# Kernel optimization log

Measured on AMD Instinct MI355X. Metric: run time of the kernel, lower is better.

## Reference

```python
import jax, jax.numpy as jnp
import numpy as np

HEADS = 8
DIM_HEAD = 64
SCALE = DIM_HEAD ** -0.5


def setup_inputs() -> dict:
    key = jax.random.key(0)
    k1, k2, k3, k4 = jax.random.split(key, 4)
    b, c, f, h, w = 2, 512, 16, 32, 32
    x = jax.random.normal(k1, (b, c, f, h, w), dtype=jnp.float32)
    pos_bias = jax.random.normal(k2, (HEADS, f, f), dtype=jnp.float32)
    # torch Linear(dim, 3*hidden, bias=False): store as (in, out) for right-matmul
    w_qkv = jax.random.normal(k3, (c, 3 * HEADS * DIM_HEAD), dtype=jnp.float32) * (c ** -0.5)
    w_out = jax.random.normal(k4, (HEADS * DIM_HEAD, c), dtype=jnp.float32) * ((HEADS * DIM_HEAD) ** -0.5)
    return {"x": x, "pos_bias": pos_bias, "w_qkv": w_qkv, "w_out": w_out}


def reference(x, pos_bias, w_qkv, w_out):
    b, c, f, h, w = x.shape
    # 'b c f h w -> (b h w) f c'
    xt = jnp.transpose(x, (0, 3, 4, 2, 1)).reshape(b * h * w, f, c)
    qkv = xt @ w_qkv  # (B, f, 3*hidden)
    q, k, v = jnp.split(qkv, 3, axis=-1)
    def to_heads(t):  # (B, f, h*d) -> (B, heads, f, d)
        return t.reshape(t.shape[0], f, HEADS, DIM_HEAD).transpose(0, 2, 1, 3)
    q, k, v = to_heads(q) * SCALE, to_heads(k), to_heads(v)
    sim = jnp.einsum('bhid,bhjd->bhij', q, k)
    sim = sim + pos_bias  # (heads, f, f) broadcasts over batch
    attn = jax.nn.softmax(sim, axis=-1)  # stable max-subtract softmax
    out = jnp.einsum('bhij,bhjd->bhid', attn, v)
    out = out.transpose(0, 2, 1, 3).reshape(b * h * w, f, HEADS * DIM_HEAD)
    out = out @ w_out  # (B, f, c)
    # '(b h w) f c -> b c f h w'
    return out.reshape(b, h, w, f, c).transpose(0, 4, 3, 1, 2)
```

## Files before the change

kernel.cpp:

```cpp
#include <hip/hip_runtime.h>

typedef unsigned short u16;
typedef unsigned int u32;
typedef __attribute__((ext_vector_type(8))) short short8;
typedef __attribute__((ext_vector_type(4))) float f32x4;

__device__ __forceinline__ u16 f2bf(float f) {
  u32 u = __builtin_bit_cast(u32, f);
  u += 0x7fffu + ((u >> 16) & 1u);
  return (u16)(u >> 16);
}

__device__ __forceinline__ void async16(const void* g, void* l) {
  __builtin_amdgcn_global_load_lds(
      (const __attribute__((address_space(1))) u32*)g,
      (__attribute__((address_space(3))) u32*)l, 16, 0, 0);
}

__global__ __launch_bounds__(256) void k_wt(const float* __restrict__ in,
                                            u16* __restrict__ outT,
                                            int K, int N, int scaleN, int perm) {
  const int bid = blockIdx.x;
  const int ntiles = N >> 5;
  const int nt = bid % ntiles, kt = bid / ntiles;
  const int n0 = nt << 5, k0 = kt << 5;
  __shared__ float tile[32][33];
  const int t = threadIdx.x;
#pragma unroll
  for (int i = 0; i < 4; ++i) {
    const int e = t + i * 256, r = e >> 5, c = e & 31;
    tile[c][r] = in[(size_t)(k0 + r) * N + n0 + c];
  }
  __syncthreads();
#pragma unroll
  for (int i = 0; i < 4; ++i) {
    const int e = t + i * 256, r = e >> 5, c = e & 31;
    float v = tile[r][c];
    if (n0 + r < scaleN) v *= 0.125f;
    const int kcol = k0 + c;
    const int kp = perm ? ((kcol & ~63) | ((kcol & 15) << 2) | ((kcol >> 4) & 3))
                        : kcol;
    outT[(size_t)(n0 + r) * K + kp] = f2bf(v);
  }
}

__global__ __launch_bounds__(256) void k_xt(const float* __restrict__ x,
                                            u16* __restrict__ XT) {
  const int bid = blockIdx.x;
  const int plane = bid & 31;
  const int rest = bid >> 5;
  const int mt = rest & 31, ct = rest >> 5;
  const int bb = plane >> 4, f = plane & 15;
  const int m0 = mt << 5, c0 = ct << 5;
  __shared__ float tile[32][33];
  const int t = threadIdx.x;
#pragma unroll
  for (int i = 0; i < 4; ++i) {
    const int e = t + i * 256, r = e >> 5, c = e & 31;
    tile[c][r] = x[((size_t)((bb * 512 + c0 + r) * 16 + f)) * 1024 + m0 + c];
  }
  __syncthreads();
#pragma unroll
  for (int i = 0; i < 4; ++i) {
    const int e = t + i * 256, r = e >> 5, c = e & 31;
    XT[((size_t)((bb * 1024 + m0 + r) * 16 + f)) * 512 + c0 + c] = f2bf(tile[r][c]);
  }
}

struct A3St { u16 A[128][64]; u16 B[192][64]; };
struct A3At { u16 q[8][16][64]; u16 k[8][16][64]; u16 vt[8][64][16]; u16 pad[16]; };
union A3Sm { A3St st; A3At at; };

__global__ __launch_bounds__(256) void k_qkv_attn(const u16* __restrict__ XT,
                                                  const u16* __restrict__ WQ,
                                                  const float* __restrict__ pos_bias,
                                                  u16* __restrict__ AO) {
  const int tid = threadIdx.x;
  const int w = tid >> 6, lane = tid & 63;
  const int c15 = lane & 15, quad = lane >> 4;
  const int bid = blockIdx.x;
  const int hd = bid & 7, m0 = (bid >> 3) << 7;

  __shared__ A3Sm sm;

  const int lr = lane >> 3, lcb = lane & 7;

  f32x4 acc[3][8];
#pragma unroll
  for (int c = 0; c < 3; ++c)
#pragma unroll
    for (int mt = 0; mt < 8; ++mt) acc[c][mt] = f32x4{0.f, 0.f, 0.f, 0.f};

  for (int kk = 0; kk < 8; ++kk) {
    __syncthreads();
    const int kc = kk << 6;
#pragma unroll
    for (int t2 = 0; t2 < 4; ++t2) {
      const int r = w * 32 + t2 * 8 + lr;
      const int swcol = kc + ((lcb ^ (r & 7)) << 3);
      async16(XT + (size_t)(m0 + r) * 512 + swcol, &sm.st.A[w * 32 + t2 * 8][0]);
    }
#pragma unroll
    for (int t2 = 0; t2 < 6; ++t2) {
      const int j = w * 48 + t2 * 8 + lr;
      const int grow = (j >> 6) * 512 + hd * 64 + (j & 63);
      const int swcol = kc + ((lcb ^ (j & 7)) << 3);
      async16(WQ + (size_t)grow * 512 + swcol, &sm.st.B[w * 48 + t2 * 8][0]);
    }
    __syncthreads();
#pragma unroll
    for (int half = 0; half < 2; ++half) {
      short8 af[8], bt[3];
#pragma unroll
      for (int mt = 0; mt < 8; ++mt) {
        const int row = mt * 16 + c15;
        const int swz = (((half << 2) + quad) ^ (row & 7)) << 3;
        af[mt] = *(const short8*)&sm.st.A[row][swz];
      }
#pragma unroll
      for (int c = 0; c < 3; ++c) {
        const int row = c * 64 + w * 16 + c15;
        const int swz = (((half << 2) + quad) ^ (row & 7)) << 3;
        bt[c] = *(const short8*)&sm.st.B[row][swz];
      }
#pragma unroll
      for (int c = 0; c < 3; ++c)
#pragma unroll
        for (int mt = 0; mt < 8; ++mt)
          acc[c][mt] = __builtin_amdgcn_mfma_f32_16x16x32_bf16(af[mt], bt[c], acc[c][mt], 0, 0, 0);
    }
  }
  __syncthreads();

  const int dloc = w * 16 + c15;
  const int ch_b = dloc >> 3, dl = dloc & 7;
#pragma unroll
  for (int mt = 0; mt < 8; ++mt) {
#pragma unroll
    for (int r = 0; r < 4; ++r) {
      const int f = quad * 4 + r;
      const int sw = ((ch_b ^ (f & 7)) << 3) | dl;
      sm.at.q[mt][f][sw] = f2bf(acc[0][mt][r]);
      sm.at.k[mt][f][sw] = f2bf(acc[1][mt][r]);
      sm.at.vt[mt][dloc][f] = f2bf(acc[2][mt][r]);
    }
  }
  __syncthreads();

  float pb[4];
#pragma unroll
  for (int r = 0; r < 4; ++r)
    pb[r] = pos_bias[hd * 256 + (quad * 4 + r) * 16 + c15];

  for (int sblk = 0; sblk < 2; ++sblk) {
    const int s = w * 2 + sblk;
    f32x4 sacc = f32x4{0.f, 0.f, 0.f, 0.f};
#pragma unroll
    for (int h = 0; h < 2; ++h) {
      const int chunk = (((h << 2) + quad) ^ (c15 & 7)) << 3;
      const short8 aq = *(const short8*)&sm.at.q[s][c15][chunk];
      const short8 bk = *(const short8*)&sm.at.k[s][c15][chunk];
      sacc = __builtin_amdgcn_mfma_f32_16x16x32_bf16(aq, bk, sacc, 0, 0, 0);
    }
    asm volatile("" ::: "memory");
    u16* lp = &sm.at.q[s][0][0];
#pragma unroll
    for (int e = 0; e < 4; ++e) lp[c15 * 32 + 16 + quad * 4 + e] = 0;
#pragma unroll
    for (int r = 0; r < 4; ++r) {
      float sv = sacc[r] + pb[r];
      float mx = sv;
      mx = fmaxf(mx, __shfl_xor(mx, 1));
      mx = fmaxf(mx, __shfl_xor(mx, 2));
      mx = fmaxf(mx, __shfl_xor(mx, 4));
      mx = fmaxf(mx, __shfl_xor(mx, 8));
      const float e = __expf(sv - mx);
      float sum = e;
      sum += __shfl_xor(sum, 1);
      sum += __shfl_xor(sum, 2);
      sum += __shfl_xor(sum, 4);
      sum += __shfl_xor(sum, 8);
      lp[(quad * 4 + r) * 32 + c15] = f2bf(e / sum);
    }
    asm volatile("" ::: "memory");
    const short8 ap = *(const short8*)&lp[c15 * 32 + quad * 8];
    f32x4 oacc[4];
#pragma unroll
    for (int t = 0; t < 4; ++t) {
      const short8 bv = *(const short8*)&sm.at.vt[s][t * 16 + c15][(quad & 1) * 8];
      oacc[t] = __builtin_amdgcn_mfma_f32_16x16x32_bf16(ap, bv, f32x4{0.f, 0.f, 0.f, 0.f}, 0, 0, 0);
    }
    const int s_g = (m0 >> 4) + s;
    const int bb = s_g >> 10, sp = s_g & 1023;
#pragma unroll
    for (int r = 0; r < 4; ++r) {
      union { u16 us[4]; uint2 v; } pk;
#pragma unroll
      for (int t = 0; t < 4; ++t) pk.us[t] = f2bf(oacc[t][r]);
      *(uint2*)(AO + ((size_t)(bb * 16384 + (quad * 4 + r) * 1024 + sp)) * 512 +
                hd * 64 + c15 * 4) = pk.v;
    }
  }
}

struct K2St { u16 A[128][64]; u16 B[128][64]; };
union K2Sm { K2St st; float C[64][130]; };

__global__ __launch_bounds__(256) void k_proj(const u16* __restrict__ AO,
                                              const u16* __restrict__ WO,
                                              float* __restrict__ out) {
  const int tid = threadIdx.x, w = tid >> 6, lane = tid & 63;
  const int c15 = lane & 15, quad = lane >> 4;
  const int bid = blockIdx.x;
  const int nb = bid & 3, mb = bid >> 2;
  const int m0 = mb << 7, n0 = nb << 7;
  const int b = m0 >> 14, mloc = m0 & 16383;
  __shared__ K2Sm sm;
  f32x4 acc[8][2];
#pragma unroll
  for (int mt = 0; mt < 8; ++mt) {
    acc[mt][0] = f32x4{0.f, 0.f, 0.f, 0.f};
    acc[mt][1] = f32x4{0.f, 0.f, 0.f, 0.f};
  }
  const int lr = lane >> 3, lcb = lane & 7;
  for (int kk = 0; kk < 8; ++kk) {
    __syncthreads();
    const int kc = kk << 6;
#pragma unroll
    for (int t2 = 0; t2 < 4; ++t2) {
      const int r = w * 32 + t2 * 8 + lr;
      const int swcol = kc + ((lcb ^ (r & 7)) << 3);
      async16(AO + (size_t)(m0 + r) * 512 + swcol, &sm.st.A[w * 32 + t2 * 8][0]);
      async16(WO + (size_t)(n0 + r) * 512 + swcol, &sm.st.B[w * 32 + t2 * 8][0]);
    }
    __syncthreads();
#pragma unroll
    for (int half = 0; half < 2; ++half) {
      short8 af[8], bt[2];
#pragma unroll
      for (int mt = 0; mt < 8; ++mt) {
        const int row = mt * 16 + c15;
        const int swz = (((half << 2) + quad) ^ (row & 7)) << 3;
        af[mt] = *(const short8*)&sm.st.A[row][swz];
      }
#pragma unroll
      for (int nt = 0; nt < 2; ++nt) {
        const int row = w * 32 + nt * 16 + c15;
        const int swz = (((half << 2) + quad) ^ (row & 7)) << 3;
        bt[nt] = *(const short8*)&sm.st.B[row][swz];
      }
#pragma unroll
      for (int mt = 0; mt < 8; ++mt) {
        acc[mt][0] = __builtin_amdgcn_mfma_f32_16x16x32_bf16(af[mt], bt[0], acc[mt][0], 0, 0, 0);
        acc[mt][1] = __builtin_amdgcn_mfma_f32_16x16x32_bf16(af[mt], bt[1], acc[mt][1], 0, 0, 0);
      }
    }
  }
  __syncthreads();
#pragma unroll
  for (int h = 0; h < 2; ++h) {
#pragma unroll
    for (int mt2 = 0; mt2 < 4; ++mt2) {
      const int mt = h * 4 + mt2;
#pragma unroll
      for (int nt = 0; nt < 2; ++nt)
#pragma unroll
        for (int r = 0; r < 4; ++r)
          sm.C[mt2 * 16 + quad * 4 + r][w * 32 + nt * 16 + c15] = acc[mt][nt][r];
    }
    __syncthreads();
    for (int jj = 0; jj < 32; ++jj) {
      const int ch = n0 + w * 32 + jj;
      out[(size_t)(b * 512 + ch) * 16384 + mloc + h * 64 + lane] = sm.C[lane][w * 32 + jj];
    }
    __syncthreads();
  }
}

extern "C" void kernel_launch(void* const* d_in, const int* in_sizes, int n_in,
                              void* d_out, int out_size, void* d_ws, size_t ws_size,
                              hipStream_t stream) {
  const float* x = (const float*)d_in[0];
  const float* pos_bias = (const float*)d_in[1];
  const float* w_qkv = (const float*)d_in[2];
  const float* w_out = (const float*)d_in[3];
  float* out = (float*)d_out;
  char* ws = (char*)d_ws;
  u16* XT = (u16*)(ws);
  u16* AO = (u16*)(ws + (size_t)33554432);
  u16* WQ = (u16*)(ws + (size_t)67108864);
  u16* WO = (u16*)(ws + (size_t)68681728);

  hipLaunchKernelGGL(k_wt, dim3(768), dim3(256), 0, stream, w_qkv, WQ, 512, 1536, 512, 0);
  hipLaunchKernelGGL(k_wt, dim3(256), dim3(256), 0, stream, w_out, WO, 512, 512, 0, 1);
  hipLaunchKernelGGL(k_xt, dim3(16384), dim3(256), 0, stream, x, XT);
  hipLaunchKernelGGL(k_qkv_attn, dim3(2048), dim3(256), 0, stream, XT, WQ, pos_bias, AO);
  hipLaunchKernelGGL(k_proj, dim3(1024), dim3(256), 0, stream, AO, WO, out);
}
```

Measured before the change: 246.2 us.

## Vectorize transpose, hoist load pointers, pack bf16 stores, reorder block indexing

The x transpose kernel now reads float4 per thread and writes packed 4-element bf16 stores instead of scalar accesses. Both GEMM kernels precompute swizzled global pointers outside the K loop and fully unroll it. V-transpose and output stores pack pairs of bf16 into 32/64-bit writes. The block-index mapping is swapped so consecutive blocks share the same head or output-column tile, changing weight reuse across concurrently running blocks. Full unrolling raises register pressure and code size.

```diff
diff --git a/kernel.cpp b/kernel.cpp
--- a/kernel.cpp
+++ b/kernel.cpp
@@ -2,6 +2,7 @@
 
 typedef unsigned short u16;
 typedef unsigned int u32;
+typedef unsigned long long u64;
 typedef __attribute__((ext_vector_type(8))) short short8;
 typedef __attribute__((ext_vector_type(4))) float f32x4;
 
@@ -9,6 +10,9 @@
   u32 u = __builtin_bit_cast(u32, f);
   u += 0x7fffu + ((u >> 16) & 1u);
   return (u16)(u >> 16);
+}
+__device__ __forceinline__ u32 pk2bf(float a, float b) {
+  return (u32)f2bf(a) | ((u32)f2bf(b) << 16);
 }
 
 __device__ __forceinline__ void async16(const void* g, void* l) {
@@ -52,19 +56,18 @@
   const int mt = rest & 31, ct = rest >> 5;
   const int bb = plane >> 4, f = plane & 15;
   const int m0 = mt << 5, c0 = ct << 5;
-  __shared__ float tile[32][33];
+  __shared__ float tile[32][36];
   const int t = threadIdx.x;
-#pragma unroll
-  for (int i = 0; i < 4; ++i) {
-    const int e = t + i * 256, r = e >> 5, c = e & 31;
-    tile[c][r] = x[((size_t)((bb * 512 + c0 + r) * 16 + f)) * 1024 + m0 + c];
-  }
-  __syncthreads();
-#pragma unroll
-  for (int i = 0; i < 4; ++i) {
-    const int e = t + i * 256, r = e >> 5, c = e & 31;
-    XT[((size_t)((bb * 1024 + m0 + r) * 16 + f)) * 512 + c0 + c] = f2bf(tile[r][c]);
-  }
+  const int lr = t >> 3, lc = t & 7;
+  const float4 v4 = *(const float4*)
+      &x[((size_t)((bb * 512 + c0 + lr) * 16 + f)) * 1024 + m0 + lc * 4];
+  *(float4*)&tile[lr][lc * 4] = v4;
+  __syncthreads();
+  const int m = t >> 3, cc = t & 7;
+  union { u32 uu[2]; u64 q; } pk;
+  pk.uu[0] = pk2bf(tile[cc * 4 + 0][m], tile[cc * 4 + 1][m]);
+  pk.uu[1] = pk2bf(tile[cc * 4 + 2][m], tile[cc * 4 + 3][m]);
+  *(u64*)&XT[((size_t)((bb * 1024 + m0 + m) * 16 + f)) * 512 + c0 + cc * 4] = pk.q;
 }
 
 struct A3St { u16 A[128][64]; u16 B[192][64]; };
@@ -79,34 +82,41 @@
   const int w = tid >> 6, lane = tid & 63;
   const int c15 = lane & 15, quad = lane >> 4;
   const int bid = blockIdx.x;
-  const int hd = bid & 7, m0 = (bid >> 3) << 7;
+  const int hd = bid >> 8, m0 = (bid & 255) << 7;
 
   __shared__ A3Sm sm;
 
   const int lr = lane >> 3, lcb = lane & 7;
 
+  const u16* aptr[4];
+  const u16* bptr[6];
+#pragma unroll
+  for (int t2 = 0; t2 < 4; ++t2) {
+    const int r = w * 32 + t2 * 8 + lr;
+    aptr[t2] = XT + (size_t)(m0 + r) * 512 + ((lcb ^ (r & 7)) << 3);
+  }
+#pragma unroll
+  for (int t2 = 0; t2 < 6; ++t2) {
+    const int j = w * 48 + t2 * 8 + lr;
+    const int grow = (j >> 6) * 512 + hd * 64 + (j & 63);
+    bptr[t2] = WQ + (size_t)grow * 512 + ((lcb ^ (j & 7)) << 3);
+  }
+
   f32x4 acc[3][8];
 #pragma unroll
   for (int c = 0; c < 3; ++c)
 #pragma unroll
     for (int mt = 0; mt < 8; ++mt) acc[c][mt] = f32x4{0.f, 0.f, 0.f, 0.f};
 
+#pragma unroll
   for (int kk = 0; kk < 8; ++kk) {
     __syncthreads();
-    const int kc = kk << 6;
-#pragma unroll
-    for (int t2 = 0; t2 < 4; ++t2) {
-      const int r = w * 32 + t2 * 8 + lr;
-      const int swcol = kc + ((lcb ^ (r & 7)) << 3);
-      async16(XT + (size_t)(m0 + r) * 512 + swcol, &sm.st.A[w * 32 + t2 * 8][0]);
-    }
-#pragma unroll
-    for (int t2 = 0; t2 < 6; ++t2) {
-      const int j = w * 48 + t2 * 8 + lr;
-      const int grow = (j >> 6) * 512 + hd * 64 + (j & 63);
-      const int swcol = kc + ((lcb ^ (j & 7)) << 3);
-      async16(WQ + (size_t)grow * 512 + swcol, &sm.st.B[w * 48 + t2 * 8][0]);
-    }
+#pragma unroll
+    for (int t2 = 0; t2 < 4; ++t2)
+      async16(aptr[t2] + (kk << 6), &sm.st.A[w * 32 + t2 * 8][0]);
+#pragma unroll
+    for (int t2 = 0; t2 < 6; ++t2)
+      async16(bptr[t2] + (kk << 6), &sm.st.B[w * 48 + t2 * 8][0]);
     __syncthreads();
 #pragma unroll
     for (int half = 0; half < 2; ++half) {
@@ -142,8 +152,11 @@
       const int sw = ((ch_b ^ (f & 7)) << 3) | dl;
       sm.at.q[mt][f][sw] = f2bf(acc[0][mt][r]);
       sm.at.k[mt][f][sw] = f2bf(acc[1][mt][r]);
-      sm.at.vt[mt][dloc][f] = f2bf(acc[2][mt][r]);
-    }
+    }
+    union { u32 uu[2]; u64 q; } pv;
+    pv.uu[0] = pk2bf(acc[2][mt][0], acc[2][mt][1]);
+    pv.uu[1] = pk2bf(acc[2][mt][2], acc[2][mt][3]);
+    *(u64*)&sm.at.vt[mt][dloc][quad * 4] = pv.q;
   }
   __syncthreads();
 
@@ -194,9 +207,9 @@
     const int bb = s_g >> 10, sp = s_g & 1023;
 #pragma unroll
     for (int r = 0; r < 4; ++r) {
-      union { u16 us[4]; uint2 v; } pk;
-#pragma unroll
-      for (int t = 0; t < 4; ++t) pk.us[t] = f2bf(oacc[t][r]);
+      union { u32 uu[2]; uint2 v; } pk;
+      pk.uu[0] = pk2bf(oacc[0][r], oacc[1][r]);
+      pk.uu[1] = pk2bf(oacc[2][r], oacc[3][r]);
       *(uint2*)(AO + ((size_t)(bb * 16384 + (quad * 4 + r) * 1024 + sp)) * 512 +
                 hd * 64 + c15 * 4) = pk.v;
     }
@@ -212,7 +225,7 @@
   const int tid = threadIdx.x, w = tid >> 6, lane = tid & 63;
   const int c15 = lane & 15, quad = lane >> 4;
   const int bid = blockIdx.x;
-  const int nb = bid & 3, mb = bid >> 2;
+  const int mb = bid & 255, nb = bid >> 8;
   const int m0 = mb << 7, n0 = nb << 7;
   const int b = m0 >> 14, mloc = m0 & 16383;
   __shared__ K2Sm sm;
@@ -223,15 +236,22 @@
     acc[mt][1] = f32x4{0.f, 0.f, 0.f, 0.f};
   }
   const int lr = lane >> 3, lcb = lane & 7;
+  const u16* aptr[4];
+  const u16* bptr[4];
+#pragma unroll
+  for (int t2 = 0; t2 < 4; ++t2) {
+    const int r = w * 32 + t2 * 8 + lr;
+    const int sw = (lcb ^ (r & 7)) << 3;
+    aptr[t2] = AO + (size_t)(m0 + r) * 512 + sw;
+    bptr[t2] = WO + (size_t)(n0 + r) * 512 + sw;
+  }
+#pragma unroll
   for (int kk = 0; kk < 8; ++kk) {
     __syncthreads();
-    const int kc = kk << 6;
 #pragma unroll
     for (int t2 = 0; t2 < 4; ++t2) {
-      const int r = w * 32 + t2 * 8 + lr;
-      const int swcol = kc + ((lcb ^ (r & 7)) << 3);
-      async16(AO + (size_t)(m0 + r) * 512 + swcol, &sm.st.A[w * 32 + t2 * 8][0]);
-      async16(WO + (size_t)(n0 + r) * 512 + swcol, &sm.st.B[w * 32 + t2 * 8][0]);
+      async16(aptr[t2] + (kk << 6), &sm.st.A[w * 32 + t2 * 8][0]);
+      async16(bptr[t2] + (kk << 6), &sm.st.B[w * 32 + t2 * 8][0]);
     }
     __syncthreads();
 #pragma unroll
```

Result: faster. 240.8 us (-2.2%).
